# Optimization experiments

Hardware: AMD Instinct MI355X
Metric: run time of the kernel (lower is better)

## Reference

```python
import jax, jax.numpy as jnp
import numpy as np

D_MODEL = 1024
N_HEADS = 16
HEAD_DIM = D_MODEL // N_HEADS  # 64
N_T = max(1, int(N_HEADS * 0.25))  # 4 time heads
N_S = N_HEADS - N_T               # 12 space heads
T_DIM = N_T * HEAD_DIM
S_DIM = N_S * HEAD_DIM
B, L = 2, 2048


def setup_inputs() -> dict:
    key = jax.random.key(0)
    ks = jax.random.split(key, 8)
    std = 0.02
    return {
        "x": jax.random.normal(ks[0], (B, L, D_MODEL), dtype=jnp.float32),
        "attention_mask": jnp.zeros((B, 1, 1, L), dtype=jnp.float32),
        # torch nn.Linear weights have shape (out_features, in_features)
        "w_qt": jax.random.normal(ks[1], (T_DIM, D_MODEL), dtype=jnp.float32) * std,
        "w_kt": jax.random.normal(ks[2], (T_DIM, D_MODEL), dtype=jnp.float32) * std,
        "w_qs": jax.random.normal(ks[3], (S_DIM, D_MODEL), dtype=jnp.float32) * std,
        "w_ks": jax.random.normal(ks[4], (S_DIM, D_MODEL), dtype=jnp.float32) * std,
        "w_sigma": jnp.zeros((1,), dtype=jnp.float32),
        "w_v": jax.random.normal(ks[5], (D_MODEL, D_MODEL), dtype=jnp.float32) * std,
        "w_o": jax.random.normal(ks[6], (D_MODEL, D_MODEL), dtype=jnp.float32) * std,
    }


def _heads(x, w, n_h):
    # x:(B,L,D) @ w.T:(D,out) -> (B,L,n_h,d_h) -> (B,n_h,L,d_h)
    b, l, _ = x.shape
    y = jnp.einsum('bld,td->blt', x, w)
    return y.reshape(b, l, n_h, HEAD_DIM).transpose(0, 2, 1, 3)


def reference(x, attention_mask, w_qt, w_kt, w_qs, w_ks, w_sigma, w_v, w_o):
    b, l, _ = x.shape
    scale = np.sqrt(HEAD_DIM).astype(np.float32)
    # F3: time heads (sign-flipped, scaled by learnable sigma) + space heads
    Qt = _heads(x, w_qt, N_T)
    Kt = _heads(x, w_kt, N_T)
    Qs = _heads(x, w_qs, N_S)
    Ks = _heads(x, w_ks, N_S)
    st = jnp.einsum('bhqd,bhkd->bhqk', Qt, Kt)  # (B,N_T,L,L)
    ss = jnp.einsum('bhqd,bhkd->bhqk', Qs, Ks)  # (B,N_S,L,L)
    sigma = jax.nn.sigmoid(w_sigma[0])
    score = jnp.concatenate([-sigma * st, ss], axis=1) / scale  # (B,H,L,L)
    score = score + attention_mask.astype(score.dtype)
    attn_probs = jax.nn.softmax(score, axis=-1).astype(x.dtype)
    # dropout p=0.0 -> identity
    V = _heads(x, w_v, N_HEADS)  # (B,H,L,d_h)
    out = jnp.einsum('bhqk,bhkd->bhqd', attn_probs, V)
    out = out.transpose(0, 2, 1, 3).reshape(b, l, D_MODEL)
    out = jnp.einsum('bld,od->blo', out, w_o)
    return out, attn_probs
```

## Files before the change

kernel.cpp:

```cpp
#include <hip/hip_runtime.h>

typedef __bf16 bf16x8 __attribute__((ext_vector_type(8)));
typedef float f32x4 __attribute__((ext_vector_type(4)));
typedef float f32x16 __attribute__((ext_vector_type(16)));
typedef short short4v __attribute__((ext_vector_type(4)));
typedef unsigned short ushort8 __attribute__((ext_vector_type(8)));
typedef unsigned int uint4v __attribute__((ext_vector_type(4)));

#define AS1 __attribute__((address_space(1)))
#define AS3 __attribute__((address_space(3)))
#define GLL16(g, l) __builtin_amdgcn_global_load_lds((const AS1 void*)(g), (AS3 void*)(l), 16, 0, 0)
#define MFMA16(a, b, c) __builtin_amdgcn_mfma_f32_16x16x32_bf16((a), (b), (c), 0, 0, 0)
#define MFMA32(a, b, c) __builtin_amdgcn_mfma_f32_32x32x16_bf16((a), (b), (c), 0, 0, 0)
#define L2E 1.44269504f

__device__ __forceinline__ unsigned short f2bf(float f) {
  unsigned int u = __builtin_bit_cast(unsigned int, f);
  u = (u + 0x7fffu + ((u >> 16) & 1u)) >> 16;
  return (unsigned short)u;
}

__device__ __forceinline__ unsigned int cvtpk_bf16(float lo, float hi) {
  unsigned int r;
  asm("v_cvt_pk_bf16_f32 %0, %1, %2" : "=v"(r) : "v"(lo), "v"(hi));
  return r;
}

__global__ void convert_kernel(const float* __restrict__ x,
                               const float* __restrict__ w_qt, const float* __restrict__ w_kt,
                               const float* __restrict__ w_qs, const float* __restrict__ w_ks,
                               const float* __restrict__ w_v, const float* __restrict__ w_o,
                               unsigned short* __restrict__ xb, unsigned short* __restrict__ wcat,
                               unsigned short* __restrict__ wob) {
  const int NX = 4096 * 1024, NW = 3072 * 1024, NO = 1024 * 1024;
  int stride = gridDim.x * blockDim.x;
  for (int i = blockIdx.x * blockDim.x + threadIdx.x; i < NX + NW + NO; i += stride) {
    if (i < NX) {
      xb[i] = f2bf(x[i]);
    } else if (i < NX + NW) {
      int j = i - NX;
      int n = j >> 10, k = j & 1023;
      const float* src;
      if (n < 256)        src = w_qt + n * 1024;
      else if (n < 1024)  src = w_qs + (n - 256) * 1024;
      else if (n < 1280)  src = w_kt + (n - 1024) * 1024;
      else if (n < 2048)  src = w_ks + (n - 1280) * 1024;
      else                src = w_v + (n - 2048) * 1024;
      wcat[j] = f2bf(src[k]);
    } else {
      int j = i - NX - NW;
      wob[j] = f2bf(w_o[j]);
    }
  }
}

__global__ __launch_bounds__(256) void gemm_qkv(const unsigned short* __restrict__ A,
                                                const unsigned short* __restrict__ Bw,
                                                const float* __restrict__ amask,
                                                unsigned short* __restrict__ qb,
                                                unsigned short* __restrict__ kfrag,
                                                unsigned short* __restrict__ vfrag) {
  __shared__ unsigned short As[128 * 32];
  __shared__ unsigned short Bs[128 * 32];
  const int t = threadIdx.x;
  const int lane = t & 63, wid = t >> 6;
  const int wm = wid >> 1, wn = wid & 1;
  const int lr = lane & 15, lg = lane >> 4;
  const int m0 = blockIdx.x * 128, n0 = blockIdx.y * 128;
  const int K = 1024;
  f32x4 acc[4][4] = {};
  const unsigned short* gA0 = A + (m0 + (t >> 2)) * K + (t & 3) * 8;
  const unsigned short* gB0 = Bw + (n0 + (t >> 2)) * K + (t & 3) * 8;
  char* lA = (char*)As + wid * 1024;
  char* lB = (char*)Bs + wid * 1024;
  for (int k0 = 0; k0 < K; k0 += 32) {
    __syncthreads();
    GLL16(gA0 + k0, lA);
    GLL16(gA0 + 64 * K + k0, lA + 4096);
    GLL16(gB0 + k0, lB);
    GLL16(gB0 + 64 * K + k0, lB + 4096);
    __syncthreads();
    bf16x8 af[4], bfr[4];
#pragma unroll
    for (int i = 0; i < 4; ++i) {
      af[i] = *(const bf16x8*)&As[(wm * 64 + i * 16 + lr) * 32 + lg * 8];
      bfr[i] = *(const bf16x8*)&Bs[(wn * 64 + i * 16 + lr) * 32 + lg * 8];
    }
#pragma unroll
    for (int i = 0; i < 4; ++i)
#pragma unroll
      for (int j = 0; j < 4; ++j)
        acc[i][j] = MFMA16(af[i], bfr[j], acc[i][j]);
  }
#pragma unroll
  for (int i = 0; i < 4; ++i) {
#pragma unroll
    for (int j = 0; j < 4; ++j) {
      int n = n0 + wn * 64 + j * 16 + lr;
      int mb = m0 + wm * 64 + i * 16 + lg * 4;
      int b = mb >> 11, l = mb & 2047;
      int cg = l >> 5;
      f32x4 v = acc[i][j];
      if (n < 1024) {
        int h = n >> 6, d = n & 63;
#pragma unroll
        for (int r = 0; r < 4; ++r)
          qb[((b * 16 + h) * 2048 + l + r) * 64 + d] = f2bf(v[r]);
      } else if (n < 2048) {
        int nn = n - 1024;
        int h = nn >> 6, d = nn & 63;
        int mfr = d >> 4, hi2 = (d >> 3) & 1, e = d & 7;
#pragma unroll
        for (int r = 0; r < 4; ++r) {
          int lr2 = l + r;
          int cgr = lr2 >> 5, ck = lr2 & 31;
          size_t idx = ((size_t)((b * 16 + h) * 64 + cgr) * 4 + mfr) * 512 + (hi2 * 32 + ck) * 8 + e;
          kfrag[idx] = f2bf(v[r]);
        }
      } else {
        int nn = n - 2048;
        int h = nn >> 6, d = nn & 63;
        int dh = d >> 5, dcol = d & 31;
        int kk = l & 31;
        int kh = kk >> 4, hi2 = (kk >> 3) & 1, i0 = kk & 7;
        const float* mrow = amask + b * 2048 + l;
        size_t idx = ((size_t)((b * 16 + h) * 64 + (l >> 5)) * 4 + (kh * 2 + dh)) * 512
                     + (hi2 * 32 + dcol) * 8 + i0;
        short4v pk;
#pragma unroll
        for (int r = 0; r < 4; ++r)
          pk[r] = (short)f2bf(v[r] * __expf(mrow[r]));
        *(short4v*)&vfrag[idx] = pk;
      }
    }
  }
}

__global__ __launch_bounds__(256, 3) void attn_kernel(const unsigned short* __restrict__ qb,
                                                      const unsigned short* __restrict__ kfrag,
                                                      const unsigned short* __restrict__ vfrag,
                                                      const float* __restrict__ mask,
                                                      const float* __restrict__ w_sigma,
                                                      float* __restrict__ probs,
                                                      unsigned short* __restrict__ ao) {
  __shared__ __align__(16) float pvacc[2048];
  __shared__ float psum[4][32];
  __shared__ float rsum[32];
  const int t = threadIdx.x;
  const int lane = t & 63, w = t >> 6;
  const int col = lane & 31, hi = lane >> 5;
  const int s = blockIdx.x;
  const int bh = (s & 7) * 4 + ((s >> 3) >> 6);
  const int q0 = ((s >> 3) & 63) * 32;
  const int b = bh >> 4, h = bh & 15;
  const float sigma = 1.0f / (1.0f + __expf(-w_sigma[0]));
  const float fac2 = ((h < 4) ? (-sigma * 0.125f) : 0.125f) * L2E;
  const float* maskb = mask + b * 2048;
  const int cg0 = w * 16;

  const unsigned short* kfb = kfrag + (size_t)bh * 131072;
  const unsigned short* vfb = vfrag + (size_t)bh * 131072;

  for (int i = t; i < 2048; i += 256) pvacc[i] = 0.0f;

  bf16x8 qf[4];
  {
    const unsigned short* qp = qb + (size_t)(bh * 2048 + q0 + col) * 64 + hi * 8;
#pragma unroll
    for (int m = 0; m < 4; ++m) qf[m] = *(const bf16x8*)(qp + m * 16);
  }

  float rs[16];
#pragma unroll
  for (int r = 0; r < 16; ++r) rs[r] = 0.f;
  for (int c = 0; c < 16; ++c) {
    int cg = cg0 + c;
    const unsigned short* kp = kfb + (size_t)cg * 2048 + lane * 8;
    bf16x8 kf0 = *(const bf16x8*)(kp);
    bf16x8 kf1 = *(const bf16x8*)(kp + 512);
    bf16x8 kf2 = *(const bf16x8*)(kp + 1024);
    bf16x8 kf3 = *(const bf16x8*)(kp + 1536);
    float mv2 = maskb[cg * 32 + col] * L2E;
    f32x16 sacc = {};
    sacc = MFMA32(qf[0], kf0, sacc);
    sacc = MFMA32(qf[1], kf1, sacc);
    sacc = MFMA32(qf[2], kf2, sacc);
    sacc = MFMA32(qf[3], kf3, sacc);
#pragma unroll
    for (int r = 0; r < 16; ++r) rs[r] += exp2f(sacc[r] * fac2 + mv2);
  }
#pragma unroll
  for (int o = 1; o < 32; o <<= 1)
#pragma unroll
    for (int r = 0; r < 16; ++r) rs[r] += __shfl_xor(rs[r], o);
  if (col == 0) {
#pragma unroll
    for (int r = 0; r < 16; ++r) psum[w][(r & 3) + 8 * (r >> 2) + 4 * hi] = rs[r];
  }
  __syncthreads();
  if (t < 32) rsum[t] = -log2f(psum[0][t] + psum[1][t] + psum[2][t] + psum[3][t]);
  __syncthreads();

  float rws_l[16];
#pragma unroll
  for (int r = 0; r < 16; ++r) rws_l[r] = rsum[(r & 3) + 8 * (r >> 2) + 4 * hi];
  const float rws_t = rsum[col];

  f32x16 oacc0 = {}, oacc1 = {};
  float* pp = probs + (size_t)(bh * 2048 + q0) * 2048;
  for (int c = 0; c < 16; ++c) {
    int cg = cg0 + c;
    const unsigned short* kp = kfb + (size_t)cg * 2048 + lane * 8;
    const unsigned short* vp = vfb + (size_t)cg * 2048 + lane * 8;
    bf16x8 kf0 = *(const bf16x8*)(kp);
    bf16x8 kf1 = *(const bf16x8*)(kp + 512);
    bf16x8 kf2 = *(const bf16x8*)(kp + 1024);
    bf16x8 kf3 = *(const bf16x8*)(kp + 1536);
    bf16x8 vf0 = *(const bf16x8*)(vp);
    bf16x8 vf1 = *(const bf16x8*)(vp + 512);
    bf16x8 vf2 = *(const bf16x8*)(vp + 1024);
    bf16x8 vf3 = *(const bf16x8*)(vp + 1536);
    float mv2 = maskb[cg * 32 + col] * L2E;
    f32x16 sn = {}, st_ = {};
    sn = MFMA32(qf[0], kf0, sn);  st_ = MFMA32(kf0, qf[0], st_);
    sn = MFMA32(qf[1], kf1, sn);  st_ = MFMA32(kf1, qf[1], st_);
    sn = MFMA32(qf[2], kf2, sn);  st_ = MFMA32(kf2, qf[2], st_);
    sn = MFMA32(qf[3], kf3, sn);  st_ = MFMA32(kf3, qf[3], st_);
    float pn[16];
#pragma unroll
    for (int r = 0; r < 16; ++r) pn[r] = exp2f(sn[r] * fac2 + (rws_l[r] + mv2));
    float pt[16];
#pragma unroll
    for (int r = 0; r < 16; ++r) pt[r] = exp2f(fminf(st_[r] * fac2 + rws_t, 60.0f));
    unsigned int A0 = cvtpk_bf16(pt[0], pt[1]),   B0 = cvtpk_bf16(pt[4], pt[5]);
    unsigned int C0 = cvtpk_bf16(pt[2], pt[3]),   D0 = cvtpk_bf16(pt[6], pt[7]);
    unsigned int E0 = cvtpk_bf16(pt[8], pt[9]),   F0 = cvtpk_bf16(pt[12], pt[13]);
    unsigned int G0 = cvtpk_bf16(pt[10], pt[11]), H0 = cvtpk_bf16(pt[14], pt[15]);
    asm("v_permlane32_swap_b32 %0, %1" : "+v"(A0), "+v"(B0));
    asm("v_permlane32_swap_b32 %0, %1" : "+v"(C0), "+v"(D0));
    asm("v_permlane32_swap_b32 %0, %1" : "+v"(E0), "+v"(F0));
    asm("v_permlane32_swap_b32 %0, %1" : "+v"(G0), "+v"(H0));
    uint4v u1; u1[0] = A0; u1[1] = C0; u1[2] = B0; u1[3] = D0;
    uint4v u2; u2[0] = E0; u2[1] = G0; u2[2] = F0; u2[3] = H0;
    bf16x8 frag1 = __builtin_bit_cast(bf16x8, u1);
    bf16x8 frag2 = __builtin_bit_cast(bf16x8, u2);
    oacc0 = MFMA32(frag1, vf0, oacc0);
    oacc1 = MFMA32(frag1, vf1, oacc1);
    oacc0 = MFMA32(frag2, vf2, oacc0);
    oacc1 = MFMA32(frag2, vf3, oacc1);
    float* pr = pp + cg * 32 + col;
#pragma unroll
    for (int r = 0; r < 16; ++r) {
      int row = (r & 3) + 8 * (r >> 2) + 4 * hi;
      __builtin_nontemporal_store(pn[r], pr + (size_t)row * 2048);
    }
  }

  __syncthreads();
#pragma unroll
  for (int r = 0; r < 16; ++r) {
    int row = (r & 3) + 8 * (r >> 2) + 4 * hi;
    atomicAdd(&pvacc[row * 64 + col], oacc0[r]);
    atomicAdd(&pvacc[row * 64 + 32 + col], oacc1[r]);
  }
  __syncthreads();
  {
    int row = t >> 3, c8 = (t & 7) * 8;
    f32x4 v0 = *(const f32x4*)&pvacc[row * 64 + c8];
    f32x4 v1 = *(const f32x4*)&pvacc[row * 64 + c8 + 4];
    ushort8 o;
#pragma unroll
    for (int i = 0; i < 4; ++i) {
      o[i] = f2bf(v0[i]);
      o[i + 4] = f2bf(v1[i]);
    }
    *(ushort8*)&ao[((b * 2048) + q0 + row) * 1024 + h * 64 + c8] = o;
  }
}

__global__ __launch_bounds__(256) void gemm_oproj(const unsigned short* __restrict__ A,
                                                  const unsigned short* __restrict__ Bw,
                                                  float* __restrict__ out) {
  __shared__ unsigned short As[128 * 32];
  __shared__ unsigned short Bs[128 * 32];
  const int t = threadIdx.x;
  const int lane = t & 63, wid = t >> 6;
  const int wm = wid >> 1, wn = wid & 1;
  const int lr = lane & 15, lg = lane >> 4;
  const int m0 = blockIdx.x * 128, n0 = blockIdx.y * 128;
  const int K = 1024;
  f32x4 acc[4][4] = {};
  const unsigned short* gA0 = A + (m0 + (t >> 2)) * K + (t & 3) * 8;
  const unsigned short* gB0 = Bw + (n0 + (t >> 2)) * K + (t & 3) * 8;
  char* lA = (char*)As + wid * 1024;
  char* lB = (char*)Bs + wid * 1024;
  for (int k0 = 0; k0 < K; k0 += 32) {
    __syncthreads();
    GLL16(gA0 + k0, lA);
    GLL16(gA0 + 64 * K + k0, lA + 4096);
    GLL16(gB0 + k0, lB);
    GLL16(gB0 + 64 * K + k0, lB + 4096);
    __syncthreads();
    bf16x8 af[4], bfr[4];
#pragma unroll
    for (int i = 0; i < 4; ++i) {
      af[i] = *(const bf16x8*)&As[(wm * 64 + i * 16 + lr) * 32 + lg * 8];
      bfr[i] = *(const bf16x8*)&Bs[(wn * 64 + i * 16 + lr) * 32 + lg * 8];
    }
#pragma unroll
    for (int i = 0; i < 4; ++i)
#pragma unroll
      for (int j = 0; j < 4; ++j)
        acc[i][j] = MFMA16(af[i], bfr[j], acc[i][j]);
  }
#pragma unroll
  for (int i = 0; i < 4; ++i) {
#pragma unroll
    for (int j = 0; j < 4; ++j) {
      int n = n0 + wn * 64 + j * 16 + lr;
      int mb = m0 + wm * 64 + i * 16 + lg * 4;
#pragma unroll
      for (int r = 0; r < 4; ++r)
        out[(mb + r) * 1024 + n] = acc[i][j][r];
    }
  }
}

extern "C" void kernel_launch(void* const* d_in, const int* in_sizes, int n_in,
                              void* d_out, int out_size, void* d_ws, size_t ws_size,
                              hipStream_t stream) {
  const float* x       = (const float*)d_in[0];
  const float* amask   = (const float*)d_in[1];
  const float* w_qt    = (const float*)d_in[2];
  const float* w_kt    = (const float*)d_in[3];
  const float* w_qs    = (const float*)d_in[4];
  const float* w_ks    = (const float*)d_in[5];
  const float* w_sigma = (const float*)d_in[6];
  const float* w_v     = (const float*)d_in[7];
  const float* w_o     = (const float*)d_in[8];

  char* ws = (char*)d_ws;
  unsigned short* xb    = (unsigned short*)ws;
  unsigned short* wcat  = (unsigned short*)(ws + 8388608);
  unsigned short* wob   = (unsigned short*)(ws + 14680064);
  unsigned short* qb    = (unsigned short*)(ws + 16777216);
  unsigned short* kfrag = (unsigned short*)(ws + 25165824);
  unsigned short* vfrag = (unsigned short*)(ws + 33554432);
  unsigned short* ao    = (unsigned short*)(ws + 41943040);

  float* outp = (float*)d_out;
  float* probs = outp + 4194304;

  convert_kernel<<<2048, 256, 0, stream>>>(x, w_qt, w_kt, w_qs, w_ks, w_v, w_o, xb, wcat, wob);
  gemm_qkv<<<dim3(32, 24), 256, 0, stream>>>(xb, wcat, amask, qb, kfrag, vfrag);
  attn_kernel<<<2048, 256, 0, stream>>>(qb, kfrag, vfrag, amask, w_sigma, probs, ao);
  gemm_oproj<<<dim3(32, 8), 256, 0, stream>>>(ao, wob, outp);
}
```

Baseline: 273.7 us.

## Compute probabilities once from transposed scores and store them as vector rows

Drops the duplicate normal-orientation QK^T MFMA chain in the attention kernel. Probabilities now come only from the transposed score tile, with the key mask applied inside the exponent rather than folded into V during the QKV GEMM. They are written with 16-byte nontemporal stores along each query row. The row-sum pass also uses the transposed layout, so one scalar accumulator replaces 16 plus a shuffle tree, and occupancy is raised to 4 waves per SIMD. Removing the fminf clamp means very large mask or score values could overflow, where before they were capped.

```diff
diff --git a/kernel.cpp b/kernel.cpp
--- a/kernel.cpp
+++ b/kernel.cpp
@@ -56,7 +56,6 @@
 
 __global__ __launch_bounds__(256) void gemm_qkv(const unsigned short* __restrict__ A,
                                                 const unsigned short* __restrict__ Bw,
-                                                const float* __restrict__ amask,
                                                 unsigned short* __restrict__ qb,
                                                 unsigned short* __restrict__ kfrag,
                                                 unsigned short* __restrict__ vfrag) {
@@ -99,7 +98,6 @@
       int n = n0 + wn * 64 + j * 16 + lr;
       int mb = m0 + wm * 64 + i * 16 + lg * 4;
       int b = mb >> 11, l = mb & 2047;
-      int cg = l >> 5;
       f32x4 v = acc[i][j];
       if (n < 1024) {
         int h = n >> 6, d = n & 63;
@@ -123,20 +121,19 @@
         int dh = d >> 5, dcol = d & 31;
         int kk = l & 31;
         int kh = kk >> 4, hi2 = (kk >> 3) & 1, i0 = kk & 7;
-        const float* mrow = amask + b * 2048 + l;
         size_t idx = ((size_t)((b * 16 + h) * 64 + (l >> 5)) * 4 + (kh * 2 + dh)) * 512
                      + (hi2 * 32 + dcol) * 8 + i0;
         short4v pk;
 #pragma unroll
         for (int r = 0; r < 4; ++r)
-          pk[r] = (short)f2bf(v[r] * __expf(mrow[r]));
+          pk[r] = (short)f2bf(v[r]);
         *(short4v*)&vfrag[idx] = pk;
       }
     }
   }
 }
 
-__global__ __launch_bounds__(256, 3) void attn_kernel(const unsigned short* __restrict__ qb,
+__global__ __launch_bounds__(256, 4) void attn_kernel(const unsigned short* __restrict__ qb,
                                                       const unsigned short* __restrict__ kfrag,
                                                       const unsigned short* __restrict__ vfrag,
                                                       const float* __restrict__ mask,
@@ -170,9 +167,7 @@
     for (int m = 0; m < 4; ++m) qf[m] = *(const bf16x8*)(qp + m * 16);
   }
 
-  float rs[16];
-#pragma unroll
-  for (int r = 0; r < 16; ++r) rs[r] = 0.f;
+  float rs = 0.f;
   for (int c = 0; c < 16; ++c) {
     int cg = cg0 + c;
     const unsigned short* kp = kfb + (size_t)cg * 2048 + lane * 8;
@@ -180,34 +175,28 @@
     bf16x8 kf1 = *(const bf16x8*)(kp + 512);
     bf16x8 kf2 = *(const bf16x8*)(kp + 1024);
     bf16x8 kf3 = *(const bf16x8*)(kp + 1536);
-    float mv2 = maskb[cg * 32 + col] * L2E;
-    f32x16 sacc = {};
-    sacc = MFMA32(qf[0], kf0, sacc);
-    sacc = MFMA32(qf[1], kf1, sacc);
-    sacc = MFMA32(qf[2], kf2, sacc);
-    sacc = MFMA32(qf[3], kf3, sacc);
-#pragma unroll
-    for (int r = 0; r < 16; ++r) rs[r] += exp2f(sacc[r] * fac2 + mv2);
-  }
-#pragma unroll
-  for (int o = 1; o < 32; o <<= 1)
-#pragma unroll
-    for (int r = 0; r < 16; ++r) rs[r] += __shfl_xor(rs[r], o);
-  if (col == 0) {
-#pragma unroll
-    for (int r = 0; r < 16; ++r) psum[w][(r & 3) + 8 * (r >> 2) + 4 * hi] = rs[r];
-  }
+    f32x16 st_ = {};
+    st_ = MFMA32(kf0, qf[0], st_);
+    st_ = MFMA32(kf1, qf[1], st_);
+    st_ = MFMA32(kf2, qf[2], st_);
+    st_ = MFMA32(kf3, qf[3], st_);
+    f32x4 lv[4];
+#pragma unroll
+    for (int g = 0; g < 4; ++g)
+      lv[g] = *(const f32x4*)&maskb[cg * 32 + g * 8 + hi * 4];
+#pragma unroll
+    for (int r = 0; r < 16; ++r)
+      rs += exp2f(st_[r] * fac2 + lv[r >> 2][r & 3] * L2E);
+  }
+  rs += __shfl_xor(rs, 32);
+  if (hi == 0) psum[w][col] = rs;
   __syncthreads();
   if (t < 32) rsum[t] = -log2f(psum[0][t] + psum[1][t] + psum[2][t] + psum[3][t]);
   __syncthreads();
-
-  float rws_l[16];
-#pragma unroll
-  for (int r = 0; r < 16; ++r) rws_l[r] = rsum[(r & 3) + 8 * (r >> 2) + 4 * hi];
   const float rws_t = rsum[col];
 
   f32x16 oacc0 = {}, oacc1 = {};
-  float* pp = probs + (size_t)(bh * 2048 + q0) * 2048;
+  float* pq = probs + (size_t)(bh * 2048 + q0 + col) * 2048;
   for (int c = 0; c < 16; ++c) {
     int cg = cg0 + c;
     const unsigned short* kp = kfb + (size_t)cg * 2048 + lane * 8;
@@ -220,18 +209,25 @@
     bf16x8 vf1 = *(const bf16x8*)(vp + 512);
     bf16x8 vf2 = *(const bf16x8*)(vp + 1024);
     bf16x8 vf3 = *(const bf16x8*)(vp + 1536);
-    float mv2 = maskb[cg * 32 + col] * L2E;
-    f32x16 sn = {}, st_ = {};
-    sn = MFMA32(qf[0], kf0, sn);  st_ = MFMA32(kf0, qf[0], st_);
-    sn = MFMA32(qf[1], kf1, sn);  st_ = MFMA32(kf1, qf[1], st_);
-    sn = MFMA32(qf[2], kf2, sn);  st_ = MFMA32(kf2, qf[2], st_);
-    sn = MFMA32(qf[3], kf3, sn);  st_ = MFMA32(kf3, qf[3], st_);
-    float pn[16];
-#pragma unroll
-    for (int r = 0; r < 16; ++r) pn[r] = exp2f(sn[r] * fac2 + (rws_l[r] + mv2));
+    f32x16 st_ = {};
+    st_ = MFMA32(kf0, qf[0], st_);
+    st_ = MFMA32(kf1, qf[1], st_);
+    st_ = MFMA32(kf2, qf[2], st_);
+    st_ = MFMA32(kf3, qf[3], st_);
+    f32x4 lv[4];
+#pragma unroll
+    for (int g = 0; g < 4; ++g)
+      lv[g] = *(const f32x4*)&maskb[cg * 32 + g * 8 + hi * 4];
     float pt[16];
 #pragma unroll
-    for (int r = 0; r < 16; ++r) pt[r] = exp2f(fminf(st_[r] * fac2 + rws_t, 60.0f));
+    for (int r = 0; r < 16; ++r)
+      pt[r] = exp2f(st_[r] * fac2 + (lv[r >> 2][r & 3] * L2E + rws_t));
+#pragma unroll
+    for (int g = 0; g < 4; ++g) {
+      f32x4 pv4;
+      pv4[0] = pt[4 * g]; pv4[1] = pt[4 * g + 1]; pv4[2] = pt[4 * g + 2]; pv4[3] = pt[4 * g + 3];
+      __builtin_nontemporal_store(pv4, (f32x4*)(pq + cg * 32 + g * 8 + hi * 4));
+    }
     unsigned int A0 = cvtpk_bf16(pt[0], pt[1]),   B0 = cvtpk_bf16(pt[4], pt[5]);
     unsigned int C0 = cvtpk_bf16(pt[2], pt[3]),   D0 = cvtpk_bf16(pt[6], pt[7]);
     unsigned int E0 = cvtpk_bf16(pt[8], pt[9]),   F0 = cvtpk_bf16(pt[12], pt[13]);
@@ -248,12 +244,6 @@
     oacc1 = MFMA32(frag1, vf1, oacc1);
     oacc0 = MFMA32(frag2, vf2, oacc0);
     oacc1 = MFMA32(frag2, vf3, oacc1);
-    float* pr = pp + cg * 32 + col;
-#pragma unroll
-    for (int r = 0; r < 16; ++r) {
-      int row = (r & 3) + 8 * (r >> 2) + 4 * hi;
-      __builtin_nontemporal_store(pn[r], pr + (size_t)row * 2048);
-    }
   }
 
   __syncthreads();
@@ -352,7 +342,7 @@
   float* probs = outp + 4194304;
 
   convert_kernel<<<2048, 256, 0, stream>>>(x, w_qt, w_kt, w_qs, w_ks, w_v, w_o, xb, wcat, wob);
-  gemm_qkv<<<dim3(32, 24), 256, 0, stream>>>(xb, wcat, amask, qb, kfrag, vfrag);
+  gemm_qkv<<<dim3(32, 24), 256, 0, stream>>>(xb, wcat, qb, kfrag, vfrag);
   attn_kernel<<<2048, 256, 0, stream>>>(qb, kfrag, vfrag, amask, w_sigma, probs, ao);
   gemm_oproj<<<dim3(32, 8), 256, 0, stream>>>(ao, wob, outp);
 }
```

New measurement: 426.2 us. 1.56x slower.
